# Kernel tuning notes

Measured on AMD Instinct MI355X. Metric: run time of the kernel, lower is better.

## Reference

```python
import jax, jax.numpy as jnp
import numpy as np

ALPHA = 0.95
BETA = 0.9

def setup_inputs() -> dict:
    key = jax.random.key(0)
    k1, k2 = jax.random.split(key)
    B, T, I, O = 64, 1000, 512, 256
    inputs = jax.random.normal(k1, (B, T, I), dtype=jnp.float32)
    W = jax.random.normal(k2, (O, I), dtype=jnp.float32) * (1.0 / np.sqrt(I))
    return {"inputs": inputs, "W": W, "nb_steps": T}

def reference(inputs, W, nb_steps):
    B = inputs.shape[0]
    O = W.shape[0]
    # linear projection: h[b,t,o]
    h = jnp.einsum('bti,oi->bto', inputs, W)
    h_t = jnp.swapaxes(h, 0, 1)  # (T, B, O) for scan over time

    def step(carry, ht):
        flt, out = carry
        new_flt = ALPHA * flt + ht
        new_out = BETA * out + flt  # uses OLD flt, matching the torch loop
        return (new_flt, new_out), new_out

    init = (jnp.zeros((B, O), jnp.float32), jnp.zeros((B, O), jnp.float32))
    _, out_rec = jax.lax.scan(step, init, h_t)
    return jnp.swapaxes(out_rec, 0, 1)  # (B, T, O)
```

## Files before the change

kernel.cpp:

```cpp
#include <hip/hip_runtime.h>
#include <hip/hip_bf16.h>
#include <stdint.h>


#define ALPHA 0.95f
#define BETA  0.9f

constexpr int Bdim = 64, T = 1000, Idim = 512, Odim = 256;
constexpr int TC = 128;
constexpr int NC = 8;
constexpr int KS = Idim / 32;
constexpr int KK = NC * KS;
constexpr int HP = 66;

typedef short bf16x8 __attribute__((ext_vector_type(8)));
typedef float f32x4  __attribute__((ext_vector_type(4)));

constexpr double dpow(double x, int n) { double r = 1; for (int i = 0; i < n; ++i) r *= x; return r; }

__device__ inline uint16_t f2bf(float a) {
  union { float f; uint32_t u; } x; x.f = a;
  return (uint16_t)((x.u + 0x7FFFu + ((x.u >> 16) & 1u)) >> 16);
}
__device__ inline float bf2f(uint16_t h) {
  union { uint32_t u; float f; } x; x.u = ((uint32_t)h) << 16; return x.f;
}

#define GLD16(g, l) __builtin_amdgcn_global_load_lds(                         \
    (const __attribute__((address_space(1))) uint32_t*)(g),                   \
    (__attribute__((address_space(3))) uint32_t*)(l), 16, 0, 0)

__device__ inline bf16x8 cvt8(float4 x0, float4 x1) {
  union { __hip_bfloat162 h[4]; bf16x8 v; } r;
  r.h[0] = __float22bfloat162_rn(make_float2(x0.x, x0.y));
  r.h[1] = __float22bfloat162_rn(make_float2(x0.z, x0.w));
  r.h[2] = __float22bfloat162_rn(make_float2(x1.x, x1.y));
  r.h[3] = __float22bfloat162_rn(make_float2(x1.z, x1.w));
  return r.v;
}

#define LGKM0 asm volatile("s_waitcnt lgkmcnt(0)" ::: "memory")
#define VMW4  asm volatile("s_waitcnt vmcnt(4)" ::: "memory")
#define SBAR  __builtin_amdgcn_s_barrier()

__global__ __launch_bounds__(512) void fused(const float* __restrict__ A,
                                             const float* __restrict__ W,
                                             float* __restrict__ Out) {
  __shared__ uint16_t Ws[64 * 512];
  __shared__ float    As[4][TC * 32];
  __shared__ uint16_t Hs[TC * HP];
  __shared__ float2   St[8][64];
  __shared__ float2   Carry[64];

  const int tid  = threadIdx.x;
  const int lane = tid & 63;
  const int w    = tid >> 6;
  const int l15  = lane & 15;
  const int quad = lane >> 4;
  const int mq   = w & 3;
  const int nh   = w >> 2;

  const int p  = blockIdx.x;
  const int b  = ((p >> 3) & 7) * 8 + (p & 7);
  const int og = p >> 6;

  const int r0 = w * 16 + (lane >> 3);
  const int g  = (lane & 7) ^ (r0 & 7);
  const float* Ab0 = A + (size_t)b * T * Idim + g * 4;

#define STAGE(kk_) do {                                                        \
    const int kc_ = (kk_); const int cc_ = kc_ >> 4, ii_ = kc_ & 15;           \
    int ra_ = cc_ * TC + r0;     if (ra_ > T - 1) ra_ = T - 1;                 \
    int rb_ = cc_ * TC + r0 + 8; if (rb_ > T - 1) rb_ = T - 1;                 \
    char* d_ = (char*)As[kc_ & 3] + w * 2048;                                  \
    GLD16(Ab0 + (size_t)ra_ * Idim + ii_ * 32, d_);                            \
    GLD16(Ab0 + (size_t)rb_ * Idim + ii_ * 32, d_ + 1024);                     \
  } while (0)

  STAGE(0); STAGE(1); STAGE(2);

  {
    const int n  = tid >> 3;
    const int s8 = tid & 7;
    const float* wp = W + (size_t)(og * 64 + n) * Idim;
#pragma unroll
    for (int rr = 0; rr < 8; ++rr) {
      int s = s8 + rr * 8;
      float4 x0 = *(const float4*)(wp + s * 8);
      float4 x1 = *(const float4*)(wp + s * 8 + 4);
      *(bf16x8*)((char*)Ws + n * 1024 + ((s ^ (n & 7)) * 16)) = cvt8(x0, x1);
    }
  }
  if (tid < 64) Carry[tid] = make_float2(0.f, 0.f);
  LGKM0; SBAR;

  constexpr float AL = (float)dpow(0.95, 16);
  constexpr float BL = (float)dpow(0.90, 16);
  constexpr float WL = (float)((dpow(0.95, 16) - dpow(0.90, 16)) / (0.95 - 0.90));

  for (int c = 0; c < NC; ++c) {
    f32x4 acc[2][2] = {};
    for (int i = 0; i < KS; ++i) {
      const int kk = c * KS + i;
      VMW4;
      SBAR;
      const float* Abuf = As[kk & 3];
      bf16x8 af[2], bfr[2];
#pragma unroll
      for (int mt = 0; mt < 2; ++mt) {
        const int m  = mq * 32 + mt * 16 + l15;
        const int s0 = (2 * quad) ^ (m & 7);
        float4 x0 = *(const float4*)&Abuf[m * 32 + s0 * 4];
        float4 x1 = *(const float4*)&Abuf[m * 32 + (s0 ^ 1) * 4];
        af[mt] = cvt8(x0, x1);
      }
#pragma unroll
      for (int nt = 0; nt < 2; ++nt) {
        const int n  = nh * 32 + nt * 16 + l15;
        const int sl = (i * 4 + quad) ^ (n & 7);
        bfr[nt] = *(const bf16x8*)((const char*)Ws + n * 1024 + sl * 16);
      }
#pragma unroll
      for (int mt = 0; mt < 2; ++mt)
#pragma unroll
        for (int nt = 0; nt < 2; ++nt)
          acc[mt][nt] = __builtin_amdgcn_mfma_f32_16x16x32_bf16(af[mt], bfr[nt], acc[mt][nt], 0, 0, 0);
      int nk = kk + 3; if (nk > KK - 1) nk = KK - 1;
      STAGE(nk);
      LGKM0;
    }

#pragma unroll
    for (int mt = 0; mt < 2; ++mt)
#pragma unroll
      for (int nt = 0; nt < 2; ++nt)
#pragma unroll
        for (int r = 0; r < 4; ++r) {
          const int tl = mq * 32 + mt * 16 + quad * 4 + r;
          const int o  = nh * 32 + nt * 16 + l15;
          Hs[tl * HP + o] = f2bf(acc[mt][nt][r]);
        }
    LGKM0; SBAR;

    {
      const int sc = w, o = lane;
      float f = 0.f, u = 0.f;
#pragma unroll
      for (int j = 0; j < 16; ++j) {
        float h = bf2f(Hs[(sc * 16 + j) * HP + o]);
        float nu = BETA * u + f; f = ALPHA * f + h; u = nu;
      }
      St[sc][o] = make_float2(f, u);
    }
    LGKM0; SBAR;

    if (tid < 64) {
      float2 cv = Carry[tid];
      float f = cv.x, u = cv.y;
#pragma unroll
      for (int cc2 = 0; cc2 < 8; ++cc2) {
        float2 s = St[cc2][tid];
        St[cc2][tid] = make_float2(f, u);
        float nu = BL * u + WL * f + s.y;
        f = AL * f + s.x;
        u = nu;
      }
      Carry[tid] = make_float2(f, u);
    }
    LGKM0; SBAR;

    {
      const int sc = w, o = lane;
      float2 s = St[sc][o];
      float f = s.x, u = s.y;
      const int tb = c * TC + sc * 16;
      float* op = Out + ((size_t)b * T + tb) * Odim + og * 64 + o;
#pragma unroll
      for (int j = 0; j < 16; ++j) {
        float h = bf2f(Hs[(sc * 16 + j) * HP + o]);
        float ov = BETA * u + f; f = ALPHA * f + h; u = ov;
        if (tb + j < T) op[j * Odim] = ov;
      }
    }
  }
#undef STAGE
}

extern "C" void kernel_launch(void* const* d_in, const int* in_sizes, int n_in,
                              void* d_out, int out_size, void* d_ws, size_t ws_size,
                              hipStream_t stream) {
  (void)in_sizes; (void)n_in; (void)d_ws; (void)ws_size; (void)out_size;
  const float* A = (const float*)d_in[0];
  const float* W = (const float*)d_in[1];
  float* Out = (float*)d_out;
  fused<<<Bdim * 4, 512, 0, stream>>>(A, W, Out);
}
```

Measured before the change: 274.5 us.

## Load A and W fragments directly into registers, drop LDS staging

Replaces the LDS-staged, async global-to-LDS pipeline for the input tile and the LDS-resident bf16 copy of W with per-lane direct global loads into registers, double-buffered two steps ahead. Each wave now fetches its own A rows and W rows from global memory every k-step. This removes the per-step barriers and LDS traffic. The H tile is kept in fp32 instead of bf16, and a trailing barrier is added per chunk. In exchange, W is re-read from global/L2 on every step and A rows are fetched redundantly by the two wave halves, which raises memory traffic and adds load latency exposure.

Measured after the change: 311.9 us. 13.6% more time.

```diff
diff --git a/kernel.cpp b/kernel.cpp
--- a/kernel.cpp
+++ b/kernel.cpp
@@ -18,18 +18,6 @@
 
 constexpr double dpow(double x, int n) { double r = 1; for (int i = 0; i < n; ++i) r *= x; return r; }
 
-__device__ inline uint16_t f2bf(float a) {
-  union { float f; uint32_t u; } x; x.f = a;
-  return (uint16_t)((x.u + 0x7FFFu + ((x.u >> 16) & 1u)) >> 16);
-}
-__device__ inline float bf2f(uint16_t h) {
-  union { uint32_t u; float f; } x; x.u = ((uint32_t)h) << 16; return x.f;
-}
-
-#define GLD16(g, l) __builtin_amdgcn_global_load_lds(                         \
-    (const __attribute__((address_space(1))) uint32_t*)(g),                   \
-    (__attribute__((address_space(3))) uint32_t*)(l), 16, 0, 0)
-
 __device__ inline bf16x8 cvt8(float4 x0, float4 x1) {
   union { __hip_bfloat162 h[4]; bf16x8 v; } r;
   r.h[0] = __float22bfloat162_rn(make_float2(x0.x, x0.y));
@@ -39,18 +27,12 @@
   return r.v;
 }
 
-#define LGKM0 asm volatile("s_waitcnt lgkmcnt(0)" ::: "memory")
-#define VMW4  asm volatile("s_waitcnt vmcnt(4)" ::: "memory")
-#define SBAR  __builtin_amdgcn_s_barrier()
-
 __global__ __launch_bounds__(512) void fused(const float* __restrict__ A,
                                              const float* __restrict__ W,
                                              float* __restrict__ Out) {
-  __shared__ uint16_t Ws[64 * 512];
-  __shared__ float    As[4][TC * 32];
-  __shared__ uint16_t Hs[TC * HP];
-  __shared__ float2   St[8][64];
-  __shared__ float2   Carry[64];
+  __shared__ float  Hs[TC * HP];
+  __shared__ float2 St[8][64];
+  __shared__ float2 Carry[64];
 
   const int tid  = threadIdx.x;
   const int lane = tid & 63;
@@ -64,35 +46,38 @@
   const int b  = ((p >> 3) & 7) * 8 + (p & 7);
   const int og = p >> 6;
 
-  const int r0 = w * 16 + (lane >> 3);
-  const int g  = (lane & 7) ^ (r0 & 7);
-  const float* Ab0 = A + (size_t)b * T * Idim + g * 4;
+  const int m0 = mq * 32 + l15;
+  const int m1 = m0 + 16;
+  const float* Abase = A + (size_t)b * T * Idim + quad * 8;
+  const float* Wp0 = W + (size_t)(og * 64 + nh * 32 + l15) * Idim + quad * 8;
+  const float* Wp1 = Wp0 + (size_t)16 * Idim;
 
-#define STAGE(kk_) do {                                                        \
-    const int kc_ = (kk_); const int cc_ = kc_ >> 4, ii_ = kc_ & 15;           \
-    int ra_ = cc_ * TC + r0;     if (ra_ > T - 1) ra_ = T - 1;                 \
-    int rb_ = cc_ * TC + r0 + 8; if (rb_ > T - 1) rb_ = T - 1;                 \
-    char* d_ = (char*)As[kc_ & 3] + w * 2048;                                  \
-    GLD16(Ab0 + (size_t)ra_ * Idim + ii_ * 32, d_);                            \
-    GLD16(Ab0 + (size_t)rb_ * Idim + ii_ * 32, d_ + 1024);                     \
+  float4 Ar[2][4];
+  float4 Wr[2][4];
+
+#define LOADA(s_, kk_) do {                                                    \
+    const int pf_ = (kk_);                                                     \
+    const int kf_ = (pf_ & 15) * 32;                                           \
+    int t0_ = (pf_ >> 4) * TC + m0; if (t0_ > T - 1) t0_ = T - 1;              \
+    int t1_ = (pf_ >> 4) * TC + m1; if (t1_ > T - 1) t1_ = T - 1;              \
+    const float* pa0_ = Abase + (size_t)t0_ * Idim + kf_;                      \
+    const float* pa1_ = Abase + (size_t)t1_ * Idim + kf_;                      \
+    Ar[s_][0] = *(const float4*)pa0_; Ar[s_][1] = *(const float4*)(pa0_ + 4);  \
+    Ar[s_][2] = *(const float4*)pa1_; Ar[s_][3] = *(const float4*)(pa1_ + 4);  \
+  } while (0)
+#define LOADW(s_, kk_) do {                                                    \
+    const int kf_ = ((kk_) & 15) * 32;                                         \
+    Wr[s_][0] = *(const float4*)(Wp0 + kf_);                                   \
+    Wr[s_][1] = *(const float4*)(Wp0 + kf_ + 4);                               \
+    Wr[s_][2] = *(const float4*)(Wp1 + kf_);                                   \
+    Wr[s_][3] = *(const float4*)(Wp1 + kf_ + 4);                               \
   } while (0)
 
-  STAGE(0); STAGE(1); STAGE(2);
+  LOADA(0, 0); LOADW(0, 0);
+  LOADA(1, 1); LOADW(1, 1);
 
-  {
-    const int n  = tid >> 3;
-    const int s8 = tid & 7;
-    const float* wp = W + (size_t)(og * 64 + n) * Idim;
-#pragma unroll
-    for (int rr = 0; rr < 8; ++rr) {
-      int s = s8 + rr * 8;
-      float4 x0 = *(const float4*)(wp + s * 8);
-      float4 x1 = *(const float4*)(wp + s * 8 + 4);
-      *(bf16x8*)((char*)Ws + n * 1024 + ((s ^ (n & 7)) * 16)) = cvt8(x0, x1);
-    }
-  }
   if (tid < 64) Carry[tid] = make_float2(0.f, 0.f);
-  LGKM0; SBAR;
+  __syncthreads();
 
   constexpr float AL = (float)dpow(0.95, 16);
   constexpr float BL = (float)dpow(0.90, 16);
@@ -100,34 +85,19 @@
 
   for (int c = 0; c < NC; ++c) {
     f32x4 acc[2][2] = {};
+#pragma unroll
     for (int i = 0; i < KS; ++i) {
-      const int kk = c * KS + i;
-      VMW4;
-      SBAR;
-      const float* Abuf = As[kk & 3];
-      bf16x8 af[2], bfr[2];
-#pragma unroll
-      for (int mt = 0; mt < 2; ++mt) {
-        const int m  = mq * 32 + mt * 16 + l15;
-        const int s0 = (2 * quad) ^ (m & 7);
-        float4 x0 = *(const float4*)&Abuf[m * 32 + s0 * 4];
-        float4 x1 = *(const float4*)&Abuf[m * 32 + (s0 ^ 1) * 4];
-        af[mt] = cvt8(x0, x1);
-      }
-#pragma unroll
-      for (int nt = 0; nt < 2; ++nt) {
-        const int n  = nh * 32 + nt * 16 + l15;
-        const int sl = (i * 4 + quad) ^ (n & 7);
-        bfr[nt] = *(const bf16x8*)((const char*)Ws + n * 1024 + sl * 16);
-      }
-#pragma unroll
-      for (int mt = 0; mt < 2; ++mt)
-#pragma unroll
-        for (int nt = 0; nt < 2; ++nt)
-          acc[mt][nt] = __builtin_amdgcn_mfma_f32_16x16x32_bf16(af[mt], bfr[nt], acc[mt][nt], 0, 0, 0);
-      int nk = kk + 3; if (nk > KK - 1) nk = KK - 1;
-      STAGE(nk);
-      LGKM0;
+      const int par = i & 1;
+      bf16x8 af0 = cvt8(Ar[par][0], Ar[par][1]);
+      bf16x8 af1 = cvt8(Ar[par][2], Ar[par][3]);
+      bf16x8 bf0 = cvt8(Wr[par][0], Wr[par][1]);
+      bf16x8 bf1 = cvt8(Wr[par][2], Wr[par][3]);
+      int pf = c * KS + i + 2; if (pf > KK - 1) pf = KK - 1;
+      LOADA(par, pf); LOADW(par, pf);
+      acc[0][0] = __builtin_amdgcn_mfma_f32_16x16x32_bf16(af0, bf0, acc[0][0], 0, 0, 0);
+      acc[0][1] = __builtin_amdgcn_mfma_f32_16x16x32_bf16(af0, bf1, acc[0][1], 0, 0, 0);
+      acc[1][0] = __builtin_amdgcn_mfma_f32_16x16x32_bf16(af1, bf0, acc[1][0], 0, 0, 0);
+      acc[1][1] = __builtin_amdgcn_mfma_f32_16x16x32_bf16(af1, bf1, acc[1][1], 0, 0, 0);
     }
 
 #pragma unroll
@@ -138,21 +108,21 @@
         for (int r = 0; r < 4; ++r) {
           const int tl = mq * 32 + mt * 16 + quad * 4 + r;
           const int o  = nh * 32 + nt * 16 + l15;
-          Hs[tl * HP + o] = f2bf(acc[mt][nt][r]);
+          Hs[tl * HP + o] = acc[mt][nt][r];
         }
-    LGKM0; SBAR;
+    __syncthreads();
 
     {
       const int sc = w, o = lane;
       float f = 0.f, u = 0.f;
 #pragma unroll
       for (int j = 0; j < 16; ++j) {
-        float h = bf2f(Hs[(sc * 16 + j) * HP + o]);
+        float h = Hs[(sc * 16 + j) * HP + o];
         float nu = BETA * u + f; f = ALPHA * f + h; u = nu;
       }
       St[sc][o] = make_float2(f, u);
     }
-    LGKM0; SBAR;
+    __syncthreads();
 
     if (tid < 64) {
       float2 cv = Carry[tid];
@@ -167,7 +137,7 @@
       }
       Carry[tid] = make_float2(f, u);
     }
-    LGKM0; SBAR;
+    __syncthreads();
 
     {
       const int sc = w, o = lane;
@@ -177,13 +147,15 @@
       float* op = Out + ((size_t)b * T + tb) * Odim + og * 64 + o;
 #pragma unroll
       for (int j = 0; j < 16; ++j) {
-        float h = bf2f(Hs[(sc * 16 + j) * HP + o]);
+        float h = Hs[(sc * 16 + j) * HP + o];
         float ov = BETA * u + f; f = ALPHA * f + h; u = ov;
         if (tb + j < T) op[j * Odim] = ov;
       }
     }
+    __syncthreads();
   }
-#undef STAGE
+#undef LOADA
+#undef LOADW
 }
 
 extern "C" void kernel_launch(void* const* d_in, const int* in_sizes, int n_in,
```
